# Performance work log

Measured on AMD Instinct MI355X. Metric: run time of the kernel, lower is better.

## Reference

```python
import jax, jax.numpy as jnp
import numpy as np


def setup_inputs() -> dict:
    key = jax.random.key(0)
    kx, kA = jax.random.split(key)
    N, d, n_neuron = 8192, 4096, 4096
    x = jax.random.normal(kx, (N, d), dtype=jnp.float32)
    A = jax.random.normal(kA, (n_neuron, d), dtype=jnp.float32) * (1.0 / np.sqrt(d))
    return {"x": x, "A": A}


def reference(x, A):
    # Ax = linear(x, A) -> [N, n_neuron]
    Ax = jnp.einsum("nd,md->nm", x, A)
    # Original forms the full [N, N] Gram matrix Ax @ Ax.T and takes its
    # diagonal; that diagonal is exactly the per-row squared norm of Ax.
    xAAx = jnp.sum(Ax * Ax, axis=1, keepdims=True)  # [N, 1]
    return xAAx
```

## Files before the change

### kernel.cpp

```cpp
#include <hip/hip_runtime.h>
#include <hip/hip_fp8.h>

typedef __bf16 bf16x8 __attribute__((ext_vector_type(8)));
typedef float  f32x4  __attribute__((ext_vector_type(4)));
typedef float  f32x16 __attribute__((ext_vector_type(16)));
typedef int    i32x4v __attribute__((ext_vector_type(4)));
typedef int    i32x8v __attribute__((ext_vector_type(8)));
typedef unsigned char uchar16v __attribute__((ext_vector_type(16)));

#define NROWS 8192
#define DK    4096
#define MCOLS 4096

#define NKT2   32
#define IMGB   32768
#define REGB   16384
#define XT2    32
#define WT2    16

#define X_BYTES ((size_t)XT2 * NKT2 * IMGB)
#define W_BYTES ((size_t)WT2 * NKT2 * IMGB)
#define WS_NEED (X_BYTES + W_BYTES)

#define BAR()  do { __builtin_amdgcn_s_barrier(); asm volatile("" ::: "memory"); } while (0)
#define LGKM0  asm volatile("s_waitcnt lgkmcnt(0)" ::: "memory")
#define VM(n)  asm volatile("s_waitcnt vmcnt(" #n ")" ::: "memory")

__device__ __forceinline__ void gload16(const unsigned char* g, unsigned char* l) {
  __builtin_amdgcn_global_load_lds(
      (const __attribute__((address_space(1))) void*)g,
      (__attribute__((address_space(3))) void*)l, 16, 0, 0);
}

__global__ __launch_bounds__(256) void convF8(const float* __restrict__ src,
                                              unsigned char* __restrict__ dst,
                                              int ntiles, float scale) {
  const int total = ntiles * 65536;
  for (int i = blockIdx.x * blockDim.x + threadIdx.x; i < total;
       i += gridDim.x * blockDim.x) {
    int lane = i & 63;
    int half = (i >> 6) & 1;
    int slot = (i >> 7) & 7;
    int ki   = (i >> 10) & 1;
    int kt   = (i >> 11) & 31;
    int tm   = i >> 16;
    int row = tm * 256 + slot * 32 + (lane & 31);
    int k   = kt * 128 + ki * 64 + (lane >> 5) * 32 + half * 16;
    const float4* p = (const float4*)(src + (size_t)row * DK + k);
    uchar16v o;
#pragma unroll
    for (int q = 0; q < 4; ++q) {
      float4 f = p[q];
      o[q * 4 + 0] = __hip_fp8_e4m3(f.x * scale).__x;
      o[q * 4 + 1] = __hip_fp8_e4m3(f.y * scale).__x;
      o[q * 4 + 2] = __hip_fp8_e4m3(f.z * scale).__x;
      o[q * 4 + 3] = __hip_fp8_e4m3(f.w * scale).__x;
    }
    *(uchar16v*)(dst + (size_t)i * 16) = o;
  }
}

__global__ __launch_bounds__(512, 2) void gemm18(const unsigned char* __restrict__ wsX,
                                                 const unsigned char* __restrict__ wsW,
                                                 float* __restrict__ out) {
  __shared__ __align__(16) unsigned char Xls[2][IMGB];
  __shared__ __align__(16) unsigned char Wls[2][IMGB];
  __shared__ float rowsum[2][256];

  const int t    = threadIdx.x;
  const int lane = t & 63;
  const int w    = t >> 6;
  const int wr4  = w >> 1;
  const int wc2  = w & 1;
  const int hi   = lane >> 5;

  unsigned bid = blockIdx.x;
  unsigned xcd = bid & 7, seq = bid >> 3;
  const int tile_m = (int)((xcd >> 1) * 8 + (seq & 7));
  const int tile_n = (int)((xcd & 1) * 8 + (seq >> 3));

  const unsigned char* xbase = wsX + (size_t)tile_m * ((size_t)NKT2 * IMGB);
  const unsigned char* wbase = wsW + (size_t)tile_n * ((size_t)NKT2 * IMGB);

  const unsigned char* pX0 = &Xls[0][0] + wr4 * 4096 + lane * 16;
  const unsigned char* pX1 = &Xls[1][0] + wr4 * 4096 + lane * 16;
  const unsigned char* pW0 = &Wls[0][0] + wc2 * 8192 + lane * 16;
  const unsigned char* pW1 = &Wls[1][0] + wc2 * 8192 + lane * 16;

  f32x16 acc[2][4] = {};
  i32x8v aP[2], aN[2], bP[2], bQ[2], bR[2], bS[2];

  auto ld32 = [&](const unsigned char* p) {
    i32x4v lo = *(const i32x4v*)p;
    i32x4v hh = *(const i32x4v*)(p + 1024);
    i32x8v r;
    r[0] = lo[0]; r[1] = lo[1]; r[2] = lo[2]; r[3] = lo[3];
    r[4] = hh[0]; r[5] = hh[1]; r[6] = hh[2]; r[7] = hh[3];
    return r;
  };

  auto readA = [&](i32x8v (&a)[2], const unsigned char* p, int ki) {
#pragma unroll
    for (int mt = 0; mt < 2; ++mt)
      a[mt] = ld32(p + ki * REGB + mt * 2048);
  };

  auto readB = [&](i32x8v (&b)[2], const unsigned char* p, int ki, int bh) {
#pragma unroll
    for (int nf2 = 0; nf2 < 2; ++nf2)
      b[nf2] = ld32(p + ki * REGB + (bh * 2 + nf2) * 2048);
  };

  auto quad = [&](const i32x8v (&a)[2], const i32x8v (&b)[2], int bh) {
    __builtin_amdgcn_s_setprio(1);
#pragma unroll
    for (int mt = 0; mt < 2; ++mt)
#pragma unroll
      for (int nf2 = 0; nf2 < 2; ++nf2)
        acc[mt][bh * 2 + nf2] = __builtin_amdgcn_mfma_scale_f32_32x32x64_f8f6f4(
            a[mt], b[nf2], acc[mt][bh * 2 + nf2],
            0, 0,
            0, 0x7F7F7F7F,
            0, 0x7F7F7F7F);
    __builtin_amdgcn_s_setprio(0);
  };

  auto stage = [&](const unsigned char* srcImg, int regionOff, unsigned char* ldsImg) {
    const unsigned char* s0 = srcImg + regionOff + t * 16;
    unsigned char* d0 = ldsImg + regionOff + w * 1024;
    gload16(s0, d0);
    gload16(s0 + 8192, d0 + 8192);
  };

  stage(xbase,         0,    &Xls[0][0]);
  stage(wbase,         0,    &Wls[0][0]);
  stage(xbase,         REGB, &Xls[0][0]);
  stage(wbase,         REGB, &Wls[0][0]);
  stage(xbase + IMGB,  0,    &Xls[1][0]);
  stage(wbase + IMGB,  0,    &Wls[1][0]);
  VM(8);
  BAR();

  for (int it = 0; it < 15; ++it) {
    const int h0 = 2 * it;
    const unsigned char* xi1 = xbase + (size_t)(h0 + 1) * IMGB;
    const unsigned char* wi1 = wbase + (size_t)(h0 + 1) * IMGB;
    const unsigned char* xi2 = xbase + (size_t)(h0 + 2) * IMGB;
    const unsigned char* wi2 = wbase + (size_t)(h0 + 2) * IMGB;
    const unsigned char* xi3 = xbase + (size_t)(h0 + 3) * IMGB;
    const unsigned char* wi3 = wbase + (size_t)(h0 + 3) * IMGB;

    readA(aP, pX0, 0); readB(bP, pW0, 0, 0); readB(bQ, pW0, 0, 1);
    stage(xi1, REGB, &Xls[1][0]);
    quad(aP, bP, 0); VM(6); BAR();
    readA(aN, pX0, 1); readB(bR, pW0, 1, 0);
    stage(wi1, REGB, &Wls[1][0]);
    quad(aP, bQ, 1); BAR();
    readB(bS, pW0, 1, 1);
    stage(xi2, 0, &Xls[0][0]);
    quad(aN, bR, 0); BAR();
    stage(wi2, 0, &Wls[0][0]);
    quad(aN, bS, 1); VM(8); BAR();

    readA(aP, pX1, 0); readB(bP, pW1, 0, 0); readB(bQ, pW1, 0, 1);
    stage(xi2, REGB, &Xls[0][0]);
    quad(aP, bP, 0); VM(6); BAR();
    readA(aN, pX1, 1); readB(bR, pW1, 1, 0);
    stage(wi2, REGB, &Wls[0][0]);
    quad(aP, bQ, 1); BAR();
    readB(bS, pW1, 1, 1);
    stage(xi3, 0, &Xls[1][0]);
    quad(aN, bR, 0); BAR();
    stage(wi3, 0, &Wls[1][0]);
    quad(aN, bS, 1); VM(8); BAR();
  }

  {
    const unsigned char* xi1 = xbase + (size_t)31 * IMGB;
    const unsigned char* wi1 = wbase + (size_t)31 * IMGB;

    readA(aP, pX0, 0); readB(bP, pW0, 0, 0);
    stage(xi1, REGB, &Xls[1][0]);
    BAR(); LGKM0; quad(aP, bP, 0); VM(6); BAR();
    readB(bQ, pW0, 0, 1);
    stage(wi1, REGB, &Wls[1][0]);
    BAR(); LGKM0; quad(aP, bQ, 1); BAR();
    readA(aN, pX0, 1); readB(bR, pW0, 1, 0);
    BAR(); LGKM0; quad(aN, bR, 0); BAR();
    readB(bS, pW0, 1, 1);
    BAR(); LGKM0; quad(aN, bS, 1); VM(4); BAR();
    readA(aP, pX1, 0); readB(bP, pW1, 0, 0);
    BAR(); LGKM0; quad(aP, bP, 0); VM(0); BAR();
    readB(bQ, pW1, 0, 1);
    BAR(); LGKM0; quad(aP, bQ, 1); BAR();
    readA(aN, pX1, 1); readB(bR, pW1, 1, 0);
    BAR(); LGKM0; quad(aN, bR, 0); BAR();
    readB(bS, pW1, 1, 1);
    LGKM0; quad(aN, bS, 1);
  }

  float v[2][16];
#pragma unroll
  for (int mt = 0; mt < 2; ++mt)
#pragma unroll
    for (int r = 0; r < 16; ++r) {
      float s = 0.f;
#pragma unroll
      for (int nf = 0; nf < 4; ++nf) {
        float c = acc[mt][nf][r];
        s += c * c;
      }
      s += __shfl_xor(s, 1, 64);
      s += __shfl_xor(s, 2, 64);
      s += __shfl_xor(s, 4, 64);
      s += __shfl_xor(s, 8, 64);
      s += __shfl_xor(s, 16, 64);
      v[mt][r] = s;
    }

  if ((lane & 31) == 0) {
#pragma unroll
    for (int mt = 0; mt < 2; ++mt)
#pragma unroll
      for (int r = 0; r < 16; ++r)
        rowsum[wc2][(wr4 * 2 + mt) * 32 + (r & 3) + 8 * (r >> 2) + 4 * hi] = v[mt][r];
  }
  __syncthreads();

  if (t < 256) {
    float p = (rowsum[0][t] + rowsum[1][t]) * (1.0f / 4096.0f);
    atomicAdd(&out[tile_m * 256 + t], p);
  }
}

__device__ __forceinline__ bf16x8 pack8(const float4& a, const float4& b) {
  bf16x8 r;
  r[0] = (__bf16)a.x; r[1] = (__bf16)a.y; r[2] = (__bf16)a.z; r[3] = (__bf16)a.w;
  r[4] = (__bf16)b.x; r[5] = (__bf16)b.y; r[6] = (__bf16)b.z; r[7] = (__bf16)b.w;
  return r;
}

struct Stage {
  float4 x0a, x0b, x1a, x1b;
  float4 a0a, a0b, a1a, a1b;
};

__global__ __launch_bounds__(256) void gemm_rowsq(const float* __restrict__ X,
                                                  const float* __restrict__ A,
                                                  float* __restrict__ out) {
  __shared__ __align__(16) __bf16 Xs[128 * 32];
  __shared__ __align__(16) __bf16 As[128 * 32];
  __shared__ float rowsum[2][128];

  const int t    = threadIdx.x;
  const int lane = t & 63;
  const int wid  = t >> 6;
  const int wr   = wid >> 1;
  const int wc   = wid & 1;
  const int l15  = lane & 15;
  const int lg   = lane >> 4;

  unsigned bid = blockIdx.x;
  unsigned swz = (bid & 7) * 256u + (bid >> 3);
  const int tile_m = swz >> 5;
  const int tile_n = swz & 31;

  const int srow = t >> 2;
  const int sc   = t & 3;
  const int cw   = sc ^ ((t >> 3) & 3);
  const int woff = srow * 32 + cw * 8;

  const float* gx = X + (size_t)(tile_m * 128 + srow) * DK + sc * 8;
  const float* ga = A + (size_t)(tile_n * 128 + srow) * DK + sc * 8;

  const int chA  = lg ^ ((l15 >> 1) & 3);
  const int aoff = (wr * 64 + l15) * 32 + chA * 8;
  const int boff = (wc * 64 + l15) * 32 + chA * 8;

  f32x4 acc[4][4] = {};

  auto load_tile = [&](int kt) {
    Stage s;
    const float* px = gx + kt * 32;
    const float* pa = ga + kt * 32;
    s.x0a = *(const float4*)(px);
    s.x0b = *(const float4*)(px + 4);
    s.x1a = *(const float4*)(px + (size_t)64 * DK);
    s.x1b = *(const float4*)(px + (size_t)64 * DK + 4);
    s.a0a = *(const float4*)(pa);
    s.a0b = *(const float4*)(pa + 4);
    s.a1a = *(const float4*)(pa + (size_t)64 * DK);
    s.a1b = *(const float4*)(pa + (size_t)64 * DK + 4);
    return s;
  };

  auto store_stage = [&](const Stage& s) {
    *(bf16x8*)(Xs + woff)            = pack8(s.x0a, s.x0b);
    *(bf16x8*)(Xs + woff + 64 * 32)  = pack8(s.x1a, s.x1b);
    *(bf16x8*)(As + woff)            = pack8(s.a0a, s.a0b);
    *(bf16x8*)(As + woff + 64 * 32)  = pack8(s.a1a, s.a1b);
  };

  auto compute = [&]() {
    bf16x8 af[4], bfr[4];
#pragma unroll
    for (int m = 0; m < 4; ++m)
      af[m] = *(const bf16x8*)(Xs + aoff + m * 16 * 32);
#pragma unroll
    for (int n = 0; n < 4; ++n)
      bfr[n] = *(const bf16x8*)(As + boff + n * 16 * 32);
#pragma unroll
    for (int m = 0; m < 4; ++m)
#pragma unroll
      for (int n = 0; n < 4; ++n)
        acc[m][n] = __builtin_amdgcn_mfma_f32_16x16x32_bf16(af[m], bfr[n],
                                                            acc[m][n], 0, 0, 0);
  };

  Stage sa = load_tile(0), sb;

  for (int kt = 0; kt < 128; kt += 2) {
    __syncthreads();
    store_stage(sa);
    sb = load_tile(kt + 1);
    __syncthreads();
    compute();
    __syncthreads();
    store_stage(sb);
    if (kt + 2 < 128) sa = load_tile(kt + 2);
    __syncthreads();
    compute();
  }

  float v[4][4];
#pragma unroll
  for (int m = 0; m < 4; ++m)
#pragma unroll
    for (int j = 0; j < 4; ++j) {
      float s = 0.f;
#pragma unroll
      for (int n = 0; n < 4; ++n) {
        float c = acc[m][n][j];
        s += c * c;
      }
      s += __shfl_xor(s, 1, 64);
      s += __shfl_xor(s, 2, 64);
      s += __shfl_xor(s, 4, 64);
      s += __shfl_xor(s, 8, 64);
      v[m][j] = s;
    }

  if (l15 == 0) {
#pragma unroll
    for (int m = 0; m < 4; ++m)
#pragma unroll
      for (int j = 0; j < 4; ++j)
        rowsum[wc][wr * 64 + m * 16 + lg * 4 + j] = v[m][j];
  }
  __syncthreads();

  if (t < 128) {
    float p = rowsum[0][t] + rowsum[1][t];
    atomicAdd(&out[tile_m * 128 + t], p);
  }
}

extern "C" void kernel_launch(void* const* d_in, const int* in_sizes, int n_in,
                              void* d_out, int out_size, void* d_ws, size_t ws_size,
                              hipStream_t stream) {
  const float* x = (const float*)d_in[0];
  const float* A = (const float*)d_in[1];
  float* out = (float*)d_out;

  hipMemsetAsync(out, 0, (size_t)out_size * sizeof(float), stream);

  if (ws_size >= WS_NEED) {
    unsigned char* wsX = (unsigned char*)d_ws;
    unsigned char* wsW = wsX + X_BYTES;
    hipLaunchKernelGGL(convF8, dim3(2048), dim3(256), 0, stream, x, wsX, XT2, 1.0f);
    hipLaunchKernelGGL(convF8, dim3(2048), dim3(256), 0, stream, A, wsW, WT2, 64.0f);
    hipLaunchKernelGGL(gemm18, dim3(512), dim3(512), 0, stream, wsX, wsW, out);
  } else {
    hipLaunchKernelGGL(gemm_rowsq, dim3(2048), dim3(256), 0, stream, x, A, out);
  }
}
```

Baseline: 158.8 us.

## Load X operand directly from global into registers, stage only W in LDS

Removes the LDS staging buffers for the X tile. Each wave now loads its X fragments straight from global memory into registers, double-buffered one k-tile ahead, while only W is staged through LDS. The old hand-tuned pipeline with partial vmcnt waits and many barriers is replaced by a simpler per-tile loop with a full vmcnt(0) wait and one barrier per tile. This cuts LDS footprint and traffic, but costs extra registers for the prefetched X fragments and exposes global latency behind a coarser wait.

```diff
diff --git a/kernel.cpp b/kernel.cpp
--- a/kernel.cpp
+++ b/kernel.cpp
@@ -23,8 +23,7 @@
 #define WS_NEED (X_BYTES + W_BYTES)
 
 #define BAR()  do { __builtin_amdgcn_s_barrier(); asm volatile("" ::: "memory"); } while (0)
-#define LGKM0  asm volatile("s_waitcnt lgkmcnt(0)" ::: "memory")
-#define VM(n)  asm volatile("s_waitcnt vmcnt(" #n ")" ::: "memory")
+#define VM0    asm volatile("s_waitcnt vmcnt(0)" ::: "memory")
 
 __device__ __forceinline__ void gload16(const unsigned char* g, unsigned char* l) {
   __builtin_amdgcn_global_load_lds(
@@ -60,10 +59,9 @@
   }
 }
 
-__global__ __launch_bounds__(512, 2) void gemm18(const unsigned char* __restrict__ wsX,
+__global__ __launch_bounds__(512, 2) void gemm19(const unsigned char* __restrict__ wsX,
                                                  const unsigned char* __restrict__ wsW,
                                                  float* __restrict__ out) {
-  __shared__ __align__(16) unsigned char Xls[2][IMGB];
   __shared__ __align__(16) unsigned char Wls[2][IMGB];
   __shared__ float rowsum[2][256];
 
@@ -82,13 +80,13 @@
   const unsigned char* xbase = wsX + (size_t)tile_m * ((size_t)NKT2 * IMGB);
   const unsigned char* wbase = wsW + (size_t)tile_n * ((size_t)NKT2 * IMGB);
 
-  const unsigned char* pX0 = &Xls[0][0] + wr4 * 4096 + lane * 16;
-  const unsigned char* pX1 = &Xls[1][0] + wr4 * 4096 + lane * 16;
+  const unsigned char* xw = xbase + wr4 * 4096 + (size_t)lane * 16;
   const unsigned char* pW0 = &Wls[0][0] + wc2 * 8192 + lane * 16;
   const unsigned char* pW1 = &Wls[1][0] + wc2 * 8192 + lane * 16;
 
   f32x16 acc[2][4] = {};
-  i32x8v aP[2], aN[2], bP[2], bQ[2], bR[2], bS[2];
+  i32x8v xa[2][2], xb[2][2];
+  i32x8v bU[2], bV[2];
 
   auto ld32 = [&](const unsigned char* p) {
     i32x4v lo = *(const i32x4v*)p;
@@ -99,10 +97,13 @@
     return r;
   };
 
-  auto readA = [&](i32x8v (&a)[2], const unsigned char* p, int ki) {
-#pragma unroll
-    for (int mt = 0; mt < 2; ++mt)
-      a[mt] = ld32(p + ki * REGB + mt * 2048);
+  auto loadXg = [&](i32x8v (&x)[2][2], int h) {
+    const unsigned char* p = xw + (size_t)h * IMGB;
+#pragma unroll
+    for (int ki = 0; ki < 2; ++ki)
+#pragma unroll
+      for (int mt = 0; mt < 2; ++mt)
+        x[ki][mt] = ld32(p + ki * REGB + mt * 2048);
   };
 
   auto readB = [&](i32x8v (&b)[2], const unsigned char* p, int ki, int bh) {
@@ -111,14 +112,14 @@
       b[nf2] = ld32(p + ki * REGB + (bh * 2 + nf2) * 2048);
   };
 
-  auto quad = [&](const i32x8v (&a)[2], const i32x8v (&b)[2], int bh) {
+  auto quad = [&](const i32x8v (&a2)[2], const i32x8v (&b)[2], int bh) {
     __builtin_amdgcn_s_setprio(1);
 #pragma unroll
     for (int mt = 0; mt < 2; ++mt)
 #pragma unroll
       for (int nf2 = 0; nf2 < 2; ++nf2)
         acc[mt][bh * 2 + nf2] = __builtin_amdgcn_mfma_scale_f32_32x32x64_f8f6f4(
-            a[mt], b[nf2], acc[mt][bh * 2 + nf2],
+            a2[mt], b[nf2], acc[mt][bh * 2 + nf2],
             0, 0,
             0, 0x7F7F7F7F,
             0, 0x7F7F7F7F);
@@ -132,71 +133,36 @@
     gload16(s0 + 8192, d0 + 8192);
   };
 
-  stage(xbase,         0,    &Xls[0][0]);
-  stage(wbase,         0,    &Wls[0][0]);
-  stage(xbase,         REGB, &Xls[0][0]);
-  stage(wbase,         REGB, &Wls[0][0]);
-  stage(xbase + IMGB,  0,    &Xls[1][0]);
-  stage(wbase + IMGB,  0,    &Wls[1][0]);
-  VM(8);
+  auto tile = [&](int h, i32x8v (&xcur)[2][2], i32x8v (&xnext)[2][2]) {
+    const unsigned char* Wcur = (h & 1) ? pW1 : pW0;
+    unsigned char* Wnxt = &Wls[(h + 1) & 1][0];
+    readB(bU, Wcur, 0, 0);
+    readB(bV, Wcur, 0, 1);
+    if (h + 1 < NKT2) {
+      loadXg(xnext, h + 1);
+      const unsigned char* wsrc = wbase + (size_t)(h + 1) * IMGB;
+      stage(wsrc, 0,    Wnxt);
+      stage(wsrc, REGB, Wnxt);
+    }
+    quad(xcur[0], bU, 0);
+    readB(bU, Wcur, 1, 0);
+    quad(xcur[0], bV, 1);
+    readB(bV, Wcur, 1, 1);
+    quad(xcur[1], bU, 0);
+    quad(xcur[1], bV, 1);
+    VM0;
+    BAR();
+  };
+
+  stage(wbase, 0,    &Wls[0][0]);
+  stage(wbase, REGB, &Wls[0][0]);
+  loadXg(xa, 0);
+  VM0;
   BAR();
 
-  for (int it = 0; it < 15; ++it) {
-    const int h0 = 2 * it;
-    const unsigned char* xi1 = xbase + (size_t)(h0 + 1) * IMGB;
-    const unsigned char* wi1 = wbase + (size_t)(h0 + 1) * IMGB;
-    const unsigned char* xi2 = xbase + (size_t)(h0 + 2) * IMGB;
-    const unsigned char* wi2 = wbase + (size_t)(h0 + 2) * IMGB;
-    const unsigned char* xi3 = xbase + (size_t)(h0 + 3) * IMGB;
-    const unsigned char* wi3 = wbase + (size_t)(h0 + 3) * IMGB;
-
-    readA(aP, pX0, 0); readB(bP, pW0, 0, 0); readB(bQ, pW0, 0, 1);
-    stage(xi1, REGB, &Xls[1][0]);
-    quad(aP, bP, 0); VM(6); BAR();
-    readA(aN, pX0, 1); readB(bR, pW0, 1, 0);
-    stage(wi1, REGB, &Wls[1][0]);
-    quad(aP, bQ, 1); BAR();
-    readB(bS, pW0, 1, 1);
-    stage(xi2, 0, &Xls[0][0]);
-    quad(aN, bR, 0); BAR();
-    stage(wi2, 0, &Wls[0][0]);
-    quad(aN, bS, 1); VM(8); BAR();
-
-    readA(aP, pX1, 0); readB(bP, pW1, 0, 0); readB(bQ, pW1, 0, 1);
-    stage(xi2, REGB, &Xls[0][0]);
-    quad(aP, bP, 0); VM(6); BAR();
-    readA(aN, pX1, 1); readB(bR, pW1, 1, 0);
-    stage(wi2, REGB, &Wls[0][0]);
-    quad(aP, bQ, 1); BAR();
-    readB(bS, pW1, 1, 1);
-    stage(xi3, 0, &Xls[1][0]);
-    quad(aN, bR, 0); BAR();
-    stage(wi3, 0, &Wls[1][0]);
-    quad(aN, bS, 1); VM(8); BAR();
-  }
-
-  {
-    const unsigned char* xi1 = xbase + (size_t)31 * IMGB;
-    const unsigned char* wi1 = wbase + (size_t)31 * IMGB;
-
-    readA(aP, pX0, 0); readB(bP, pW0, 0, 0);
-    stage(xi1, REGB, &Xls[1][0]);
-    BAR(); LGKM0; quad(aP, bP, 0); VM(6); BAR();
-    readB(bQ, pW0, 0, 1);
-    stage(wi1, REGB, &Wls[1][0]);
-    BAR(); LGKM0; quad(aP, bQ, 1); BAR();
-    readA(aN, pX0, 1); readB(bR, pW0, 1, 0);
-    BAR(); LGKM0; quad(aN, bR, 0); BAR();
-    readB(bS, pW0, 1, 1);
-    BAR(); LGKM0; quad(aN, bS, 1); VM(4); BAR();
-    readA(aP, pX1, 0); readB(bP, pW1, 0, 0);
-    BAR(); LGKM0; quad(aP, bP, 0); VM(0); BAR();
-    readB(bQ, pW1, 0, 1);
-    BAR(); LGKM0; quad(aP, bQ, 1); BAR();
-    readA(aN, pX1, 1); readB(bR, pW1, 1, 0);
-    BAR(); LGKM0; quad(aN, bR, 0); BAR();
-    readB(bS, pW1, 1, 1);
-    LGKM0; quad(aN, bS, 1);
+  for (int h = 0; h < NKT2; h += 2) {
+    tile(h,     xa, xb);
+    tile(h + 1, xb, xa);
   }
 
   float v[2][16];
@@ -379,7 +345,7 @@
     unsigned char* wsW = wsX + X_BYTES;
     hipLaunchKernelGGL(convF8, dim3(2048), dim3(256), 0, stream, x, wsX, XT2, 1.0f);
     hipLaunchKernelGGL(convF8, dim3(2048), dim3(256), 0, stream, A, wsW, WT2, 64.0f);
-    hipLaunchKernelGGL(gemm18, dim3(512), dim3(512), 0, stream, wsX, wsW, out);
+    hipLaunchKernelGGL(gemm19, dim3(512), dim3(512), 0, stream, wsX, wsW, out);
   } else {
     hipLaunchKernelGGL(gemm_rowsq, dim3(2048), dim3(256), 0, stream, x, A, out);
   }
```

After: 555.1 us. +249.5%, slower.
